# Kernel optimization log

Hardware: AMD Instinct MI355X
Metric: run time of the kernel (lower is better)

Reference implementation:

```python
import jax, jax.numpy as jnp
import numpy as np

KH = KW = 3
SH = SW = 1
DH = DW = 1

def _same_padding(ih, iw):
    eff_kh = (KH - 1) * DH + 1
    eff_kw = (KW - 1) * DW + 1
    out_h = (ih + SH - 1) // SH
    out_w = (iw + SW - 1) // SW
    pad_h = max((out_h - 1) * SH + eff_kh - ih, 0)
    pad_w = max((out_w - 1) * SW + eff_kw - iw, 0)
    pad_top = pad_h // 2
    pad_bottom = pad_h - pad_top
    pad_left = pad_w // 2
    pad_right = pad_w - pad_left
    return (pad_top, pad_bottom), (pad_left, pad_right)


def setup_inputs() -> dict:
    key = jax.random.key(0)
    k1, k2, k3 = jax.random.split(key, 3)
    N, C, H, Wd = 32, 192, 56, 56
    Cout = 384
    x = jax.random.normal(k1, (N, C, H, Wd), dtype=jnp.float32)
    # linear weight (Cout, C*KH*KW) with unfold ordering (c, kh, kw) -> OIHW kernel
    W = jax.random.normal(k2, (Cout, C, KH, KW), dtype=jnp.float32) * (1.0 / np.sqrt(C * KH * KW))
    b = jax.random.normal(k3, (Cout,), dtype=jnp.float32) * 0.01
    return {"x": x, "W": W, "b": b}


def reference(x, W, b):
    # ConvLayer: F.pad('same') -> nn.Unfold -> Linear -> reshape, which is
    # mathematically a 2D conv with OIHW kernel W (unfold orders features as c,kh,kw).
    _, _, H, Wd = x.shape
    pad_hw = _same_padding(H, Wd)
    out = jax.lax.conv_general_dilated(
        x, W,
        window_strides=(SH, SW),
        padding=pad_hw,
        rhs_dilation=(DH, DW),
        dimension_numbers=("NCHW", "OIHW", "NCHW"),
    )
    return out + b[None, :, None, None]
```

## Files before the change

### kernel.cpp

```cpp
#include <hip/hip_runtime.h>
#include <cstdint>
#include <cstddef>

#define N_IMG 32
#define C_IN 192
#define HW 56
#define SPAT 3136
#define C_OUT 384
#define HP 58
#define KPOS 9
#define KTOT 1728
#define NT 27

#define BM 128
#define BN 256
#define NT_CO 3
#define NT_S  392
#define GRID_MAIN (NT_CO*NT_S)

#define BUF_EL 24576
#define B_BASE 8192

typedef __attribute__((ext_vector_type(8))) short short8;
typedef __attribute__((ext_vector_type(4))) float f32x4;

__device__ __forceinline__ unsigned short f2bf(float f) {
  union { float f; unsigned u; } v; v.f = f;
  unsigned u = v.u;
  unsigned r = (u + 0x7FFFu + ((u >> 16) & 1u)) >> 16;
  return (unsigned short)r;
}

__device__ __forceinline__ void async_load16(const void* gsrc, void* ldst) {
  __builtin_amdgcn_global_load_lds(
      (const __attribute__((address_space(1))) unsigned int*)gsrc,
      (__attribute__((address_space(3))) unsigned int*)ldst,
      16, 0, 0);
}

__device__ __forceinline__ void vm0() { asm volatile("s_waitcnt vmcnt(0)" ::: "memory"); }
#define SBAR0() __builtin_amdgcn_sched_barrier(0)

__global__ void pack_w(const float* __restrict__ W, unsigned short* __restrict__ Wp) {
  int idx = blockIdx.x*256 + threadIdx.x;
  if (idx >= C_OUT*KPOS*C_IN) return;
  int c   = idx % C_IN;
  int pos = (idx / C_IN) % KPOS;
  int co  = idx / (C_IN*KPOS);
  float v = W[((size_t)co*C_IN + c)*KPOS + pos];
  Wp[idx] = f2bf(v);
}

__global__ void zero_border(unsigned short* __restrict__ Xp) {
  int idx = blockIdx.x*256 + threadIdx.x;
  if (idx >= N_IMG*228*C_IN) return;
  int c    = idx % C_IN;
  int cell = (idx / C_IN) % 228;
  int n    = idx / (C_IN*228);
  int hh, ww;
  if (cell < 116) { hh = (cell < 58) ? 0 : 57; ww = cell % 58; }
  else { int b2 = cell - 116; ww = (b2 < 56) ? 0 : 57; hh = 1 + (b2 % 56); }
  Xp[(((size_t)n*HP + hh)*HP + ww)*C_IN + c] = 0;
}

__global__ void pack_x(const float* __restrict__ x, unsigned short* __restrict__ Xp) {
  __shared__ float tile[64*57];
  int b  = blockIdx.x;
  int cb = b % 3;
  int h  = (b/3) % HW;
  int n  = b / (3*HW);
  int tid = threadIdx.x;
  const float* src = x + (size_t)n*C_IN*SPAT + (size_t)cb*64*SPAT + h*HW;
  #pragma unroll
  for (int i = 0; i < 14; ++i) {
    int idx = i*256 + tid;
    int c = idx / HW, w = idx % HW;
    tile[c*57 + w] = src[(size_t)c*SPAT + w];
  }
  __syncthreads();
  unsigned short* dst = Xp + (((size_t)n*HP + h + 1)*HP + 1)*C_IN + cb*64;
  #pragma unroll
  for (int i = 0; i < 14; ++i) {
    int idx = i*256 + tid;
    int w = idx / 64, c = idx % 64;
    dst[(size_t)w*C_IN + c] = f2bf(tile[c*57 + w]);
  }
}

__global__ __launch_bounds__(512, 2) void conv_gemm(
    const unsigned short* __restrict__ Wp,
    const unsigned short* __restrict__ Xp,
    const float* __restrict__ bias,
    float* __restrict__ out)
{
  __shared__ __attribute__((aligned(16))) unsigned short lds[3][BUF_EL];

  int bid = blockIdx.x;
  int wg = (bid & 7) * (GRID_MAIN/8) + (bid >> 3);
  int cotile = wg % NT_CO;
  int stile  = wg / NT_CO;

  const int tid   = threadIdx.x;
  const int lane  = tid & 63;
  const int wv    = tid >> 6;
  const int wm    = wv >> 2;
  const int wn    = wv & 3;
  const int lanep = lane & 15;
  const int laneq = lane >> 4;
  const int l3    = lane >> 3;
  const int l7    = lane & 7;
  const int gsl   = (l7 ^ l3) << 3;

  const unsigned short* aSrc0 = Wp + (size_t)(cotile*BM + wv*8      + l3)*KTOT + gsl;
  const unsigned short* aSrc1 = Wp + (size_t)(cotile*BM + (wv+8)*8  + l3)*KTOT + gsl;
  const int aOff0 = wv*512;
  const int aOff1 = (wv+8)*512;

  const unsigned short* bSrc[4];
  int bOff[4];
  #pragma unroll
  for (int i = 0; i < 4; ++i) {
    int cbk = i*8 + wv;
    int rb  = cbk*8 + l3;
    int f   = stile*BN + rb;
    int n   = f / SPAT, sp = f % SPAT;
    bSrc[i] = Xp + (((size_t)n*HP + sp/HW)*HP + sp%HW)*C_IN + gsl;
    bOff[i] = B_BASE + cbk*512;
  }

  const int aRd = (wm*64 + lanep)*64 + ((laneq ^ (lanep & 7)) << 3);
  const int bRd = B_BASE + (wn*64 + lanep)*64 + ((laneq ^ (lanep & 7)) << 3);

  f32x4 acc[4][4];
  #pragma unroll
  for (int mf = 0; mf < 4; ++mf)
    #pragma unroll
    for (int nf = 0; nf < 4; ++nf)
      acc[mf][nf] = (f32x4){0.f, 0.f, 0.f, 0.f};

  auto bOffOf = [](int t) {
    int pos = t / 3;
    int c0  = (t - pos*3) * 64;
    int kh  = pos / 3, kw = pos - kh*3;
    return (kh*HP + kw)*C_IN + c0;
  };

  auto stage = [&](int t, unsigned short* base) {
    const int koff = t*64;
    async_load16(aSrc0 + koff, base + aOff0);
    async_load16(aSrc1 + koff, base + aOff1);
    const int bo = bOffOf(t);
    #pragma unroll
    for (int i = 0; i < 4; ++i)
      async_load16(bSrc[i] + bo, base + bOff[i]);
  };

  short8 pA0[4], pB0[4], pA1[4], pB1[4];

#define PHASE(BC, BNX, RCA, RCB, RNA, RNB, DO_NEXT, STAGE_STMT, DO_BAR)     \
  {                                                                         \
    const unsigned short* bc_ = (BC);                                       \
    const unsigned short* bn_ = (BNX);                                      \
    short8 a1_[4], b1_[4];                                                  \
    _Pragma("unroll")                                                       \
    for (int mf = 0; mf < 4; ++mf) a1_[mf] = *(const short8*)&bc_[(aRd + mf*1024) ^ 32]; \
    _Pragma("unroll")                                                       \
    for (int nf = 0; nf < 4; ++nf) b1_[nf] = *(const short8*)&bc_[(bRd + nf*1024) ^ 32]; \
    if (DO_NEXT) {                                                          \
      _Pragma("unroll")                                                     \
      for (int mf = 0; mf < 4; ++mf) RNA[mf] = *(const short8*)&bn_[aRd + mf*1024]; \
      _Pragma("unroll")                                                     \
      for (int nf = 0; nf < 4; ++nf) RNB[nf] = *(const short8*)&bn_[bRd + nf*1024]; \
    }                                                                       \
    STAGE_STMT;                                                             \
    SBAR0();                                                                \
    __builtin_amdgcn_s_setprio(1);                                          \
    _Pragma("unroll")                                                       \
    for (int mf = 0; mf < 4; ++mf)                                          \
      _Pragma("unroll")                                                     \
      for (int nf = 0; nf < 4; ++nf)                                        \
        acc[mf][nf] = __builtin_amdgcn_mfma_f32_16x16x32_bf16(              \
            RCA[mf], RCB[nf], acc[mf][nf], 0, 0, 0);                        \
    _Pragma("unroll")                                                       \
    for (int mf = 0; mf < 4; ++mf)                                          \
      _Pragma("unroll")                                                     \
      for (int nf = 0; nf < 4; ++nf)                                        \
        acc[mf][nf] = __builtin_amdgcn_mfma_f32_16x16x32_bf16(              \
            a1_[mf], b1_[nf], acc[mf][nf], 0, 0, 0);                        \
    __builtin_amdgcn_s_setprio(0);                                          \
    SBAR0();                                                                \
    if (DO_BAR) {                                                           \
      vm0();                                                                \
      __builtin_amdgcn_s_barrier();                                         \
      SBAR0();                                                              \
    }                                                                       \
  }

  unsigned short* b0 = &lds[0][0];
  unsigned short* b1 = &lds[1][0];
  unsigned short* b2 = &lds[2][0];

  stage(0, b0);
  stage(1, b1);
  vm0();
  __builtin_amdgcn_s_barrier();
  SBAR0();
  #pragma unroll
  for (int mf = 0; mf < 4; ++mf) pA0[mf] = *(const short8*)&b0[aRd + mf*1024];
  #pragma unroll
  for (int nf = 0; nf < 4; ++nf) pB0[nf] = *(const short8*)&b0[bRd + nf*1024];

  for (int t0 = 0; t0 < 24; t0 += 6) {
    PHASE(b0, b1, pA0, pB0, pA1, pB1, true, (stage(t0 + 2, b2)), true);
    PHASE(b1, b2, pA1, pB1, pA0, pB0, true, (stage(t0 + 3, b0)), true);
    PHASE(b2, b0, pA0, pB0, pA1, pB1, true, (stage(t0 + 4, b1)), true);
    PHASE(b0, b1, pA1, pB1, pA0, pB0, true, (stage(t0 + 5, b2)), true);
    PHASE(b1, b2, pA0, pB0, pA1, pB1, true, (stage(t0 + 6, b0)), true);
    PHASE(b2, b0, pA1, pB1, pA0, pB0, true, (stage(t0 + 7, b1)), true);
  }
  PHASE(b0, b1, pA0, pB0, pA1, pB1, true, (stage(26, b2)), true);
  PHASE(b1, b2, pA1, pB1, pA0, pB0, true, (void)0, true);
  PHASE(b2, b0, pA0, pB0, pA1, pB1, false, (void)0, false);
#undef PHASE

  const int coB = cotile*BM + wm*64;
  const int fB  = stile*BN + wn*64;
  #pragma unroll
  for (int nf = 0; nf < 4; ++nf) {
    int f  = fB + nf*16 + lanep;
    int n  = f / SPAT;
    int sp = f % SPAT;
    float* obase = out + (size_t)n*C_OUT*SPAT + sp;
    #pragma unroll
    for (int mf = 0; mf < 4; ++mf) {
      #pragma unroll
      for (int i = 0; i < 4; ++i) {
        int co = coB + mf*16 + laneq*4 + i;
        obase[(size_t)co*SPAT] = acc[mf][nf][i] + bias[co];
      }
    }
  }
}

__global__ void conv_naive(const float* __restrict__ x, const float* __restrict__ W,
                           const float* __restrict__ bias, float* __restrict__ out) {
  size_t idx = (size_t)blockIdx.x*256 + threadIdx.x;
  if (idx >= (size_t)N_IMG*C_OUT*SPAT) return;
  int s  = idx % SPAT;
  int co = (int)((idx / SPAT) % C_OUT);
  int n  = (int)(idx / ((size_t)SPAT*C_OUT));
  int h = s / HW, w = s % HW;
  float acc = bias[co];
  for (int c = 0; c < C_IN; ++c)
    for (int kh = 0; kh < 3; ++kh) {
      int hh = h + kh - 1;
      if (hh < 0 || hh >= HW) continue;
      for (int kw = 0; kw < 3; ++kw) {
        int ww = w + kw - 1;
        if (ww < 0 || ww >= HW) continue;
        acc += x[(((size_t)n*C_IN + c)*HW + hh)*HW + ww]
             * W[(((size_t)co*C_IN + c)*3 + kh)*3 + kw];
      }
    }
  out[idx] = acc;
}

extern "C" void kernel_launch(void* const* d_in, const int* in_sizes, int n_in,
                              void* d_out, int out_size, void* d_ws, size_t ws_size,
                              hipStream_t stream) {
  const float* x = (const float*)d_in[0];
  const float* W = (const float*)d_in[1];
  const float* b = (const float*)d_in[2];
  float* out = (float*)d_out;

  const size_t WP_ELEMS = (size_t)C_OUT*KTOT;
  const size_t XP_ELEMS = (size_t)N_IMG*HP*HP*C_IN;
  const size_t NEED = (WP_ELEMS + XP_ELEMS)*2;

  if (ws_size >= NEED) {
    unsigned short* Wp = (unsigned short*)d_ws;
    unsigned short* Xp = Wp + WP_ELEMS;
    zero_border<<<(N_IMG*228*C_IN + 255)/256, 256, 0, stream>>>(Xp);
    pack_w<<<(int)((WP_ELEMS + 255)/256), 256, 0, stream>>>(W, Wp);
    pack_x<<<N_IMG*HW*3, 256, 0, stream>>>(x, Xp);
    conv_gemm<<<GRID_MAIN, 512, 0, stream>>>(Wp, Xp, b, out);
  } else {
    size_t total = (size_t)N_IMG*C_OUT*SPAT;
    conv_naive<<<(int)((total + 255)/256), 256, 0, stream>>>(x, W, b, out);
  }
}
```

Before: 169.7 us.

## Load activation fragments directly from global into registers, bypassing LDS

```diff
diff --git a/kernel.cpp b/kernel.cpp
--- a/kernel.cpp
+++ b/kernel.cpp
@@ -18,8 +18,7 @@
 #define NT_S  392
 #define GRID_MAIN (NT_CO*NT_S)
 
-#define BUF_EL 24576
-#define B_BASE 8192
+#define BUF_EL 8192
 
 typedef __attribute__((ext_vector_type(8))) short short8;
 typedef __attribute__((ext_vector_type(4))) float f32x4;
@@ -38,6 +37,7 @@
       16, 0, 0);
 }
 
+__device__ __forceinline__ void vm2() { asm volatile("s_waitcnt vmcnt(2)" ::: "memory"); }
 __device__ __forceinline__ void vm0() { asm volatile("s_waitcnt vmcnt(0)" ::: "memory"); }
 #define SBAR0() __builtin_amdgcn_sched_barrier(0)
 
@@ -116,20 +116,15 @@
   const int aOff0 = wv*512;
   const int aOff1 = (wv+8)*512;
 
-  const unsigned short* bSrc[4];
-  int bOff[4];
-  #pragma unroll
-  for (int i = 0; i < 4; ++i) {
-    int cbk = i*8 + wv;
-    int rb  = cbk*8 + l3;
-    int f   = stile*BN + rb;
-    int n   = f / SPAT, sp = f % SPAT;
-    bSrc[i] = Xp + (((size_t)n*HP + sp/HW)*HP + sp%HW)*C_IN + gsl;
-    bOff[i] = B_BASE + cbk*512;
+  const unsigned short* bFrag[4];
+  #pragma unroll
+  for (int nf = 0; nf < 4; ++nf) {
+    int f  = stile*BN + wn*64 + nf*16 + lanep;
+    int n  = f / SPAT, sp = f % SPAT;
+    bFrag[nf] = Xp + (((size_t)n*HP + sp/HW)*HP + sp%HW)*C_IN + laneq*8;
   }
 
   const int aRd = (wm*64 + lanep)*64 + ((laneq ^ (lanep & 7)) << 3);
-  const int bRd = B_BASE + (wn*64 + lanep)*64 + ((laneq ^ (lanep & 7)) << 3);
 
   f32x4 acc[4][4];
   #pragma unroll
@@ -149,29 +144,27 @@
     const int koff = t*64;
     async_load16(aSrc0 + koff, base + aOff0);
     async_load16(aSrc1 + koff, base + aOff1);
-    const int bo = bOffOf(t);
-    #pragma unroll
-    for (int i = 0; i < 4; ++i)
-      async_load16(bSrc[i] + bo, base + bOff[i]);
   };
 
-  short8 pA0[4], pB0[4], pA1[4], pB1[4];
-
-#define PHASE(BC, BNX, RCA, RCB, RNA, RNB, DO_NEXT, STAGE_STMT, DO_BAR)     \
+  short8 bA[8], bB[8];
+
+#define PHASE(LB, CUR, NXT, DO_B, T1, STAGE_STMT, VM_STMT, DO_BAR)          \
   {                                                                         \
-    const unsigned short* bc_ = (BC);                                       \
-    const unsigned short* bn_ = (BNX);                                      \
-    short8 a1_[4], b1_[4];                                                  \
-    _Pragma("unroll")                                                       \
-    for (int mf = 0; mf < 4; ++mf) a1_[mf] = *(const short8*)&bc_[(aRd + mf*1024) ^ 32]; \
-    _Pragma("unroll")                                                       \
-    for (int nf = 0; nf < 4; ++nf) b1_[nf] = *(const short8*)&bc_[(bRd + nf*1024) ^ 32]; \
-    if (DO_NEXT) {                                                          \
+    const unsigned short* lb_ = (LB);                                       \
+    short8 a0_[4], a1_[4];                                                  \
+    _Pragma("unroll")                                                       \
+    for (int mf = 0; mf < 4; ++mf) a0_[mf] = *(const short8*)&lb_[aRd + mf*1024];        \
+    _Pragma("unroll")                                                       \
+    for (int mf = 0; mf < 4; ++mf) a1_[mf] = *(const short8*)&lb_[(aRd + mf*1024) ^ 32]; \
+    if (DO_B) {                                                             \
+      const int bo_ = bOffOf(T1);                                           \
       _Pragma("unroll")                                                     \
-      for (int mf = 0; mf < 4; ++mf) RNA[mf] = *(const short8*)&bn_[aRd + mf*1024]; \
-      _Pragma("unroll")                                                     \
-      for (int nf = 0; nf < 4; ++nf) RNB[nf] = *(const short8*)&bn_[bRd + nf*1024]; \
+      for (int kk = 0; kk < 2; ++kk)                                        \
+        _Pragma("unroll")                                                   \
+        for (int nf = 0; nf < 4; ++nf)                                      \
+          NXT[kk*4+nf] = *(const short8*)(bFrag[nf] + bo_ + kk*32);         \
     }                                                                       \
+    SBAR0();                                                                \
     STAGE_STMT;                                                             \
     SBAR0();                                                                \
     __builtin_amdgcn_s_setprio(1);                                          \
@@ -180,17 +173,17 @@
       _Pragma("unroll")                                                     \
       for (int nf = 0; nf < 4; ++nf)                                        \
         acc[mf][nf] = __builtin_amdgcn_mfma_f32_16x16x32_bf16(              \
-            RCA[mf], RCB[nf], acc[mf][nf], 0, 0, 0);                        \
+            a0_[mf], CUR[nf], acc[mf][nf], 0, 0, 0);                        \
     _Pragma("unroll")                                                       \
     for (int mf = 0; mf < 4; ++mf)                                          \
       _Pragma("unroll")                                                     \
       for (int nf = 0; nf < 4; ++nf)                                        \
         acc[mf][nf] = __builtin_amdgcn_mfma_f32_16x16x32_bf16(              \
-            a1_[mf], b1_[nf], acc[mf][nf], 0, 0, 0);                        \
+            a1_[mf], CUR[4+nf], acc[mf][nf], 0, 0, 0);                      \
     __builtin_amdgcn_s_setprio(0);                                          \
     SBAR0();                                                                \
+    VM_STMT;                                                                \
     if (DO_BAR) {                                                           \
-      vm0();                                                                \
       __builtin_amdgcn_s_barrier();                                         \
       SBAR0();                                                              \
     }                                                                       \
@@ -202,25 +195,29 @@
 
   stage(0, b0);
   stage(1, b1);
+  {
+    const int bo_ = bOffOf(0);
+    #pragma unroll
+    for (int kk = 0; kk < 2; ++kk)
+      #pragma unroll
+      for (int nf = 0; nf < 4; ++nf)
+        bA[kk*4+nf] = *(const short8*)(bFrag[nf] + bo_ + kk*32);
+  }
   vm0();
   __builtin_amdgcn_s_barrier();
   SBAR0();
-  #pragma unroll
-  for (int mf = 0; mf < 4; ++mf) pA0[mf] = *(const short8*)&b0[aRd + mf*1024];
-  #pragma unroll
-  for (int nf = 0; nf < 4; ++nf) pB0[nf] = *(const short8*)&b0[bRd + nf*1024];
 
   for (int t0 = 0; t0 < 24; t0 += 6) {
-    PHASE(b0, b1, pA0, pB0, pA1, pB1, true, (stage(t0 + 2, b2)), true);
-    PHASE(b1, b2, pA1, pB1, pA0, pB0, true, (stage(t0 + 3, b0)), true);
-    PHASE(b2, b0, pA0, pB0, pA1, pB1, true, (stage(t0 + 4, b1)), true);
-    PHASE(b0, b1, pA1, pB1, pA0, pB0, true, (stage(t0 + 5, b2)), true);
-    PHASE(b1, b2, pA0, pB0, pA1, pB1, true, (stage(t0 + 6, b0)), true);
-    PHASE(b2, b0, pA1, pB1, pA0, pB0, true, (stage(t0 + 7, b1)), true);
-  }
-  PHASE(b0, b1, pA0, pB0, pA1, pB1, true, (stage(26, b2)), true);
-  PHASE(b1, b2, pA1, pB1, pA0, pB0, true, (void)0, true);
-  PHASE(b2, b0, pA0, pB0, pA1, pB1, false, (void)0, false);
+    PHASE(b0, bA, bB, true, t0+1, (stage(t0+2, b2)), vm2(), true);
+    PHASE(b1, bB, bA, true, t0+2, (stage(t0+3, b0)), vm2(), true);
+    PHASE(b2, bA, bB, true, t0+3, (stage(t0+4, b1)), vm2(), true);
+    PHASE(b0, bB, bA, true, t0+4, (stage(t0+5, b2)), vm2(), true);
+    PHASE(b1, bA, bB, true, t0+5, (stage(t0+6, b0)), vm2(), true);
+    PHASE(b2, bB, bA, true, t0+6, (stage(t0+7, b1)), vm2(), true);
+  }
+  PHASE(b0, bA, bB, true, 25, (stage(26, b2)), vm2(), true);
+  PHASE(b1, bB, bA, true, 26, (void)0, vm0(), true);
+  PHASE(b2, bA, bB, false, 0, (void)0, (void)0, false);
 #undef PHASE
 
   const int coB = cotile*BM + wm*64;
```

Result: slower. 344.8 us (+103.3%).
